# Performance work log

Hardware: AMD Instinct MI355X
Metric: run time of the kernel (lower is better)

The kernel has to match this reference:

```python
import jax, jax.numpy as jnp
import numpy as np

N = 50000        # nodes
E = 400000       # edges (avg degree 8)
F_IN = 128       # num_features
HID = 64         # hidden_channels
H = 4            # num_heads
D = HID // H     # headc = 16
C = 16           # num_classes
K_HOPS = 3
ALPHA = 0.1
CST = 1e-5


def setup_inputs() -> dict:
    key = jax.random.key(0)
    ks = jax.random.split(key, 16)
    s = 0.05
    x = jax.random.normal(ks[0], (N, F_IN), dtype=jnp.float32)
    edge_index = jax.random.randint(ks[1], (2, E), 0, N, dtype=jnp.int64)
    Wi = jax.random.normal(ks[2], (F_IN, HID), dtype=jnp.float32) * s
    bi = jnp.zeros((HID,), dtype=jnp.float32)
    Wq = jax.random.normal(ks[3], (HID, H * D), dtype=jnp.float32) * s
    bq = jnp.zeros((H * D,), dtype=jnp.float32)
    Wk = jax.random.normal(ks[4], (HID, H * D), dtype=jnp.float32) * s
    bk = jnp.zeros((H * D,), dtype=jnp.float32)
    Wv = jax.random.normal(ks[5], (HID, H * C), dtype=jnp.float32) * s
    bv = jnp.zeros((H * C,), dtype=jnp.float32)
    Wo = jax.random.normal(ks[6], (H * C, C), dtype=jnp.float32) * s
    bo = jnp.zeros((C,), dtype=jnp.float32)
    # hopwise/temp init as in the torch module (ind_gamma=True, gamma_softmax=True)
    hw = ALPHA * (1.0 - ALPHA) ** np.arange(K_HOPS + 1)
    hw[-1] = (1.0 - ALPHA) ** K_HOPS
    hopwise = jnp.asarray(hw, dtype=jnp.float32)
    temp = jax.random.uniform(ks[7], (H, K_HOPS + 1), dtype=jnp.float32)
    return {"x": x, "edge_index": edge_index, "Wi": Wi, "bi": bi, "Wq": Wq,
            "bq": bq, "Wk": Wk, "bk": bk, "Wv": Wv, "bv": bv, "Wo": Wo,
            "bo": bo, "hopwise": hopwise, "temp": temp}


def reference(x, edge_index, Wi, bi, Wq, bq, Wk, bk, Wv, bv, Wo, bo, hopwise, temp):
    # dropout p=0 (inference); input transform + relu
    h = jax.nn.relu(x @ Wi + bi)                       # (N, HID)
    Q = (1.0 + jax.nn.elu(h @ Wq + bq)).reshape(N, H, D)
    Kt = (1.0 + jax.nn.elu(h @ Wk + bk)).reshape(N, H, D)
    V = (h @ Wv + bv).reshape(N, H, C)
    M = jnp.einsum('nhi,nhj->nhij', Kt, V)             # (N, H, D, C)
    hidden = V * temp[:, 0][None, :, None]             # hop-0 term
    # NB: torch F.softmax(temp, dim=-2) normalizes over the HEAD axis
    layerwise = jax.nn.softmax(temp, axis=0)           # (H, K+1)
    src, dst = edge_index[0], edge_index[1]
    for hop in range(K_HOPS):
        M = jax.ops.segment_sum(M[src], dst, num_segments=N)
        Kt = jax.ops.segment_sum(Kt[src], dst, num_segments=N)
        Hm = jnp.einsum('nhi,nhij->nhj', Q, M)         # (N, H, C)
        den = jnp.einsum('nhi,nhi->nh', Q, Kt)[..., None] + CST
        gamma = hopwise[hop + 1] * layerwise[:, hop + 1][:, None]  # (H, 1)
        hidden = hidden + gamma * (Hm / den)
    # multi_concat=True path
    out = hidden.reshape(N, H * C) @ Wo + bo           # (N, C)
    return out
```

## Files before the change

kernel.cpp:

```cpp
#include <hip/hip_runtime.h>
#include <math.h>

#define F_IN 128
#define HID  64
#define NH   4
#define DD   16
#define CC   16
#define CSTE 1e-5f

typedef _Float16 h2     __attribute__((ext_vector_type(2)));
typedef float    f2     __attribute__((ext_vector_type(2)));
typedef short    short8 __attribute__((ext_vector_type(8)));
typedef float    f4v    __attribute__((ext_vector_type(4)));

#define WIT_LD 136
#define W2T_LD 72
#define H_LD   72

__device__ __forceinline__ unsigned short bf16r(float f) {
    unsigned int u = __builtin_bit_cast(unsigned int, f);
    unsigned int r = (u + 0x7FFFu + ((u >> 16) & 1u)) >> 16;
    return (unsigned short)r;
}

__device__ __forceinline__ int uni(int v) {
    return __builtin_amdgcn_readfirstlane(v);
}

__device__ __forceinline__ float fp8_to_f32(unsigned int b) {
    f2 v = __builtin_amdgcn_cvt_pk_f32_fp8((int)b, false);
    return v.x;
}
__device__ __forceinline__ f2 fp8x2_to_f32(unsigned int w) {
    return __builtin_amdgcn_cvt_pk_f32_fp8((int)w, false);
}
__device__ __forceinline__ f2 fp8x2_to_f32_hi(unsigned int w) {
    return __builtin_amdgcn_cvt_pk_f32_fp8((int)w, true);
}
__device__ __forceinline__ unsigned char f32_to_fp8(float f) {
    int w = __builtin_amdgcn_cvt_pk_fp8_f32(f, f, 0, false);
    return (unsigned char)(w & 0xff);
}

__device__ __forceinline__ float fp4_dec1(unsigned int n) {
    unsigned int e = (n >> 1) & 3u, m = n & 1u;
    float mag = (e == 0) ? 0.5f * (float)m
                         : (float)(1u << (e - 1)) * (1.0f + 0.5f * (float)m);
    return (n & 8u) ? -mag : mag;
}
__device__ __forceinline__ unsigned int fp4_enc1(float f) {
    unsigned int s = (f < 0.f) ? 8u : 0u;
    float a = fabsf(f);
    unsigned int m;
    if      (a < 0.25f) m = 0u;
    else if (a < 0.75f) m = 1u;
    else if (a < 1.25f) m = 2u;
    else if (a < 1.75f) m = 3u;
    else if (a < 2.5f)  m = 4u;
    else if (a < 3.5f)  m = 5u;
    else if (a < 5.0f)  m = 6u;
    else                m = 7u;
    return s | m;
}

#if __has_builtin(__builtin_amdgcn_cvt_scalef32_pk_f32_fp4) && __has_builtin(__builtin_amdgcn_cvt_scalef32_pk_fp4_f32)
#define HAS_FP4 1
#endif

__device__ __forceinline__ void fp4x16_dec2(uint2 w, f2* v) {
#ifdef HAS_FP4
    v[0] = __builtin_amdgcn_cvt_scalef32_pk_f32_fp4(w.x, 1.0f, 0);
    v[1] = __builtin_amdgcn_cvt_scalef32_pk_f32_fp4(w.x, 1.0f, 1);
    v[2] = __builtin_amdgcn_cvt_scalef32_pk_f32_fp4(w.x, 1.0f, 2);
    v[3] = __builtin_amdgcn_cvt_scalef32_pk_f32_fp4(w.x, 1.0f, 3);
    v[4] = __builtin_amdgcn_cvt_scalef32_pk_f32_fp4(w.y, 1.0f, 0);
    v[5] = __builtin_amdgcn_cvt_scalef32_pk_f32_fp4(w.y, 1.0f, 1);
    v[6] = __builtin_amdgcn_cvt_scalef32_pk_f32_fp4(w.y, 1.0f, 2);
    v[7] = __builtin_amdgcn_cvt_scalef32_pk_f32_fp4(w.y, 1.0f, 3);
#else
    #pragma unroll
    for (int j = 0; j < 4; ++j) {
        v[j].x     = fp4_dec1((w.x >> (8 * j)) & 0xFu);
        v[j].y     = fp4_dec1((w.x >> (8 * j + 4)) & 0xFu);
        v[4 + j].x = fp4_dec1((w.y >> (8 * j)) & 0xFu);
        v[4 + j].y = fp4_dec1((w.y >> (8 * j + 4)) & 0xFu);
    }
#endif
}

__device__ __forceinline__ uint2 fp4x16_enc(const float* v) {
#ifdef HAS_FP4
    unsigned int a = 0u, b = 0u;
    a = __builtin_amdgcn_cvt_scalef32_pk_fp4_f32(a, v[0],  v[1],  1.0f, 0);
    a = __builtin_amdgcn_cvt_scalef32_pk_fp4_f32(a, v[2],  v[3],  1.0f, 1);
    a = __builtin_amdgcn_cvt_scalef32_pk_fp4_f32(a, v[4],  v[5],  1.0f, 2);
    a = __builtin_amdgcn_cvt_scalef32_pk_fp4_f32(a, v[6],  v[7],  1.0f, 3);
    b = __builtin_amdgcn_cvt_scalef32_pk_fp4_f32(b, v[8],  v[9],  1.0f, 0);
    b = __builtin_amdgcn_cvt_scalef32_pk_fp4_f32(b, v[10], v[11], 1.0f, 1);
    b = __builtin_amdgcn_cvt_scalef32_pk_fp4_f32(b, v[12], v[13], 1.0f, 2);
    b = __builtin_amdgcn_cvt_scalef32_pk_fp4_f32(b, v[14], v[15], 1.0f, 3);
    return {a, b};
#else
    unsigned int a = 0u, b = 0u;
    #pragma unroll
    for (int j = 0; j < 8; ++j) {
        a |= fp4_enc1(v[j])     << (4 * j);
        b |= fp4_enc1(v[8 + j]) << (4 * j);
    }
    return {a, b};
#endif
}

__device__ __forceinline__ void store_m_row(
    uint2* __restrict__ Mout, unsigned short* __restrict__ SKout,
    int node, int lane, const float* u, float kacc)
{
    float rm = 0.f;
    #pragma unroll
    for (int j = 0; j < 16; ++j) rm = fmaxf(rm, fabsf(u[j]));
    unsigned char s8 = f32_to_fp8(rm * (1.0f / 6.0f));
    float se = fp8_to_f32((unsigned int)s8);
    float invs = (se > 0.f) ? (1.0f / se) : 0.f;
    float tq[16];
    #pragma unroll
    for (int j = 0; j < 16; ++j) tq[j] = u[j] * invs;
    Mout[(size_t)node * 64 + lane] = fp4x16_enc(tq);
    SKout[(size_t)node * 64 + lane] =
        (unsigned short)((unsigned short)s8 | ((unsigned short)f32_to_fp8(kacc) << 8));
}

__device__ __forceinline__ float gamma_for(const float* __restrict__ temp,
                                           const float* __restrict__ hopwise,
                                           int h, int hop) {
    float t0 = temp[0 * 4 + hop], t1 = temp[1 * 4 + hop];
    float t2 = temp[2 * 4 + hop], t3 = temp[3 * 4 + hop];
    float mx = fmaxf(fmaxf(t0, t1), fmaxf(t2, t3));
    float e0 = __expf(t0 - mx), e1 = __expf(t1 - mx);
    float e2 = __expf(t2 - mx), e3 = __expf(t3 - mx);
    float ssum = e0 + e1 + e2 + e3;
    float eh = (h == 0) ? e0 : (h == 1) ? e1 : (h == 2) ? e2 : e3;
    return hopwise[hop] * eh / ssum;
}

__device__ __forceinline__ void reduce_scatter16(float* u, int p) {
    #pragma unroll
    for (int k = 0; k < 4; ++k) {
        const int m = 1 << k;
        bool bit = (p >> k) & 1;
        const int n = 8 >> k;
        #pragma unroll
        for (int j = 0; j < n; ++j) {
            float give = bit ? u[2 * j]     : u[2 * j + 1];
            float keep = bit ? u[2 * j + 1] : u[2 * j];
            float got  = __shfl_xor(give, m, 64);
            u[j] = keep + got;
        }
    }
}

__device__ __forceinline__ float den16(float qd, float kacc) {
    float kq = qd * kacc;
    kq += __shfl_xor(kq, 1, 64);
    kq += __shfl_xor(kq, 2, 64);
    kq += __shfl_xor(kq, 4, 64);
    kq += __shfl_xor(kq, 8, 64);
    return kq + CSTE;
}

__device__ __forceinline__ void acc_edge23(f2* u2, float& kacc,
                                           uint2 w, unsigned int skraw) {
    f2 sk = fp8x2_to_f32(skraw);
    kacc += sk.y;
    f2 v[8];
    fp4x16_dec2(w, v);
    f2 s = {sk.x, sk.x};
    #pragma unroll
    for (int j = 0; j < 8; ++j) u2[j] = s * v[j] + u2[j];
}

__device__ __forceinline__ void acc_edge1(f2* u2, float& kacc,
                                          uint4 vw, unsigned int kraw) {
    float kk = fp8_to_f32(kraw);
    kacc += kk;
    f2 v[8];
    v[0] = fp8x2_to_f32(vw.x);  v[1] = fp8x2_to_f32_hi(vw.x);
    v[2] = fp8x2_to_f32(vw.y);  v[3] = fp8x2_to_f32_hi(vw.y);
    v[4] = fp8x2_to_f32(vw.z);  v[5] = fp8x2_to_f32_hi(vw.z);
    v[6] = fp8x2_to_f32(vw.w);  v[7] = fp8x2_to_f32_hi(vw.w);
    f2 s = {kk, kk};
    #pragma unroll
    for (int j = 0; j < 8; ++j) u2[j] = s * v[j] + u2[j];
}

__global__ __launch_bounds__(1024) void scan_a(const int* __restrict__ deg,
                                               int* __restrict__ offsets,
                                               int* __restrict__ bsum, int N) {
    __shared__ int wsum[16], woff[16];
    int lane = threadIdx.x & 63, w = threadIdx.x >> 6;
    int i0 = blockIdx.x * 4096 + (int)threadIdx.x * 4;
    int d0 = (i0 + 0 < N) ? deg[i0 + 0] : 0;
    int d1 = (i0 + 1 < N) ? deg[i0 + 1] : 0;
    int d2 = (i0 + 2 < N) ? deg[i0 + 2] : 0;
    int d3 = (i0 + 3 < N) ? deg[i0 + 3] : 0;
    int tsum = d0 + d1 + d2 + d3;
    int incl = tsum;
    #pragma unroll
    for (int m = 1; m < 64; m <<= 1) {
        int t = __shfl_up(incl, m, 64);
        if (lane >= m) incl += t;
    }
    if (lane == 63) wsum[w] = incl;
    __syncthreads();
    if (threadIdx.x == 0) {
        int r = 0;
        for (int k = 0; k < 16; ++k) { int t = wsum[k]; woff[k] = r; r += t; }
        bsum[blockIdx.x] = r;
    }
    __syncthreads();
    int excl = woff[w] + incl - tsum;
    if (i0 + 0 < N) offsets[i0 + 0] = excl;
    if (i0 + 1 < N) offsets[i0 + 1] = excl + d0;
    if (i0 + 2 < N) offsets[i0 + 2] = excl + d0 + d1;
    if (i0 + 3 < N) offsets[i0 + 3] = excl + d0 + d1 + d2;
}

__global__ void scan_c(int* __restrict__ offsets, const int* __restrict__ bsum,
                       int nb, int N) {
    int i = blockIdx.x * blockDim.x + threadIdx.x;
    if (i < N) {
        int bkt = i >> 12;
        int base = 0;
        for (int b = 0; b < bkt; ++b) base += bsum[b];
        offsets[i] += base;
    }
    if (i == 0) {
        int tot = 0;
        for (int b = 0; b < nb; ++b) tot += bsum[b];
        offsets[N] = tot;
    }
}

__global__ void scatter_kernel(const int* __restrict__ ei, const int* __restrict__ offsets,
                               int* __restrict__ cursor, int* __restrict__ csr, int E) {
    int e = blockIdx.x * blockDim.x + threadIdx.x;
    if (e < E) {
        int src = ei[e];
        int dst = ei[E + e];
        int pos = atomicAdd(&cursor[dst], 1);
        csr[offsets[dst] + pos] = src;
    }
}

__global__ __launch_bounds__(256) void qkv_count(
    const float* __restrict__ x,
    const float* __restrict__ Wi, const float* __restrict__ bi,
    const float* __restrict__ Wq, const float* __restrict__ bq,
    const float* __restrict__ Wk, const float* __restrict__ bk,
    const float* __restrict__ Wv, const float* __restrict__ bv,
    float* __restrict__ Q, unsigned char* __restrict__ VKq,
    _Float16* __restrict__ Vh,
    const int* __restrict__ ei, int* __restrict__ deg,
    int E, int qb, int N)
{
    __shared__ unsigned short wit[64 * WIT_LD];
    __shared__ unsigned short w2t[192 * W2T_LD];
    __shared__ unsigned short hlds[64 * H_LD];
    if ((int)blockIdx.x >= qb) {
        int e = ((int)blockIdx.x - qb) * 256 + (int)threadIdx.x;
        if (e < E) atomicAdd(&deg[ei[E + e]], 1);
        return;
    }
    int t = threadIdx.x;
    #pragma unroll
    for (int i = 0; i < 32; ++i) {
        int g = t + i * 256;
        wit[(g & 63) * WIT_LD + (g >> 6)] = bf16r(Wi[g]);
    }
    #pragma unroll
    for (int i = 0; i < 16; ++i) {
        int g = t + i * 256;
        int k = g >> 6, n = g & 63;
        w2t[(n      ) * W2T_LD + k] = bf16r(Wq[g]);
        w2t[(n +  64) * W2T_LD + k] = bf16r(Wk[g]);
        w2t[(n + 128) * W2T_LD + k] = bf16r(Wv[g]);
    }
    __syncthreads();

    int lane = t & 63, w = t >> 6;
    int p = lane & 15, quad = lane >> 4;
    int mbase = blockIdx.x * 64 + w * 16;

    short8 afrag[4];
    {
        int node = mbase + p;
        if (node >= N) node = N - 1;
        const float* xr = x + (size_t)node * F_IN + quad * 8;
        #pragma unroll
        for (int ks = 0; ks < 4; ++ks) {
            float4 a0 = *(const float4*)(xr + ks * 32);
            float4 a1 = *(const float4*)(xr + ks * 32 + 4);
            short8 f;
            f[0] = bf16r(a0.x); f[1] = bf16r(a0.y); f[2] = bf16r(a0.z); f[3] = bf16r(a0.w);
            f[4] = bf16r(a1.x); f[5] = bf16r(a1.y); f[6] = bf16r(a1.z); f[7] = bf16r(a1.w);
            afrag[ks] = f;
        }
    }
    #pragma unroll
    for (int nt = 0; nt < 4; ++nt) {
        f4v acc = {0.f, 0.f, 0.f, 0.f};
        #pragma unroll
        for (int ks = 0; ks < 4; ++ks) {
            short8 b = *(const short8*)&wit[(nt * 16 + p) * WIT_LD + ks * 32 + quad * 8];
            acc = __builtin_amdgcn_mfma_f32_16x16x32_bf16(afrag[ks], b, acc, 0, 0, 0);
        }
        float bb = bi[nt * 16 + p];
        #pragma unroll
        for (int r = 0; r < 4; ++r) {
            float hv = fmaxf(acc[r] + bb, 0.f);
            hlds[(w * 16 + quad * 4 + r) * H_LD + nt * 16 + p] = bf16r(hv);
        }
    }
    __syncthreads();

    short8 ha0 = *(const short8*)&hlds[(w * 16 + p) * H_LD + quad * 8];
    short8 ha1 = *(const short8*)&hlds[(w * 16 + p) * H_LD + 32 + quad * 8];
    int node_r = mbase + quad * 4;
    #pragma unroll
    for (int nt = 0; nt < 12; ++nt) {
        f4v acc = {0.f, 0.f, 0.f, 0.f};
        short8 b0 = *(const short8*)&w2t[(nt * 16 + p) * W2T_LD + quad * 8];
        short8 b1 = *(const short8*)&w2t[(nt * 16 + p) * W2T_LD + 32 + quad * 8];
        acc = __builtin_amdgcn_mfma_f32_16x16x32_bf16(ha0, b0, acc, 0, 0, 0);
        acc = __builtin_amdgcn_mfma_f32_16x16x32_bf16(ha1, b1, acc, 0, 0, 0);
        int col = nt * 16 + p;
        #pragma unroll
        for (int r = 0; r < 4; ++r) {
            int node = node_r + r;
            if (node >= N) continue;
            float v = acc[r];
            if (col < 64) {
                v += bq[col];
                Q[(size_t)node * 64 + col] = (v > 0.f) ? (1.f + v) : __expf(v);
            } else if (col < 128) {
                int c = col - 64;
                v += bk[c];
                float kv = (v > 0.f) ? (1.f + v) : __expf(v);
                VKq[(size_t)node * 128 + 64 + c] = f32_to_fp8(kv);
            } else {
                int c = col - 128;
                v += bv[c];
                Vh[(size_t)node * 64 + c] = (_Float16)v;
                VKq[(size_t)node * 128 + c] = f32_to_fp8(v);
            }
        }
    }
}


__global__ __launch_bounds__(256) void hop1_all(
    const float* __restrict__ Q, const unsigned char* __restrict__ VKq,
    const _Float16* __restrict__ Vh,
    const int* __restrict__ offsets, const int* __restrict__ csr,
    const float* __restrict__ temp, const float* __restrict__ hopwise,
    uint2* __restrict__ M1, unsigned short* __restrict__ SK1,
    float* __restrict__ hidden, int N)
{
    int lane = threadIdx.x & 63;
    int node = blockIdx.x * 4 + (threadIdx.x >> 6);
    if (node >= N) return;
    int h = lane >> 4;
    float gh = gamma_for(temp, hopwise, h, 1);
    float h0 = (float)Vh[(size_t)node * 64 + lane] * temp[h * 4];
    float qd = Q[(size_t)node * 64 + lane];
    f2 u2[8];
    #pragma unroll
    for (int j = 0; j < 8; ++j) u2[j] = f2{0.f, 0.f};
    float kacc = 0.f;
    int beg = uni(offsets[node]), end = uni(offsets[node + 1]);
    int t = beg;
    for (; t + 3 < end; t += 4) {
        int s0 = uni(csr[t]),     s1 = uni(csr[t + 1]);
        int s2 = uni(csr[t + 2]), s3 = uni(csr[t + 3]);
        const unsigned char* b0 = VKq + (size_t)s0 * 128;
        const unsigned char* b1 = VKq + (size_t)s1 * 128;
        const unsigned char* b2 = VKq + (size_t)s2 * 128;
        const unsigned char* b3 = VKq + (size_t)s3 * 128;
        uint4 v0 = *(const uint4*)(b0 + h * 16);
        uint4 v1 = *(const uint4*)(b1 + h * 16);
        uint4 v2 = *(const uint4*)(b2 + h * 16);
        uint4 v3 = *(const uint4*)(b3 + h * 16);
        unsigned char k0 = b0[64 + lane];
        unsigned char k1 = b1[64 + lane];
        unsigned char k2 = b2[64 + lane];
        unsigned char k3 = b3[64 + lane];
        acc_edge1(u2, kacc, v0, k0);
        acc_edge1(u2, kacc, v1, k1);
        acc_edge1(u2, kacc, v2, k2);
        acc_edge1(u2, kacc, v3, k3);
    }
    for (; t < end; ++t) {
        int s = uni(csr[t]);
        const unsigned char* b = VKq + (size_t)s * 128;
        uint4 vw = *(const uint4*)(b + h * 16);
        unsigned char kk = b[64 + lane];
        acc_edge1(u2, kacc, vw, kk);
    }
    float u[16];
    #pragma unroll
    for (int j = 0; j < 8; ++j) { u[2 * j] = u2[j].x; u[2 * j + 1] = u2[j].y; }
    store_m_row(M1, SK1, node, lane, u, kacc);
    #pragma unroll
    for (int j = 0; j < 16; ++j) u[j] *= qd;
    reduce_scatter16(u, lane & 15);
    float g = gh / den16(qd, kacc);
    hidden[(size_t)node * 64 + lane] = h0 + g * u[0];
}

template<bool STORE>
__global__ __launch_bounds__(256) void hop23_all(
    const float* __restrict__ Q, const uint2* __restrict__ Mprev,
    const unsigned short* __restrict__ SKprev,
    const int* __restrict__ offsets, const int* __restrict__ csr,
    const float* __restrict__ temp, const float* __restrict__ hopwise,
    uint2* __restrict__ Mnext, unsigned short* __restrict__ SKnext,
    float* __restrict__ hidden,
    const float* __restrict__ Wo, const float* __restrict__ bo,
    float* __restrict__ out, int N, int hop)
{
    int lane = threadIdx.x & 63;
    int node = blockIdx.x * 4 + (threadIdx.x >> 6);
    if (node >= N) return;
    float gh = gamma_for(temp, hopwise, lane >> 4, hop);
    float qd  = Q[(size_t)node * 64 + lane];
    float hv0 = STORE ? 0.f : hidden[(size_t)node * 64 + lane];
    f2 u2[8];
    #pragma unroll
    for (int j = 0; j < 8; ++j) u2[j] = f2{0.f, 0.f};
    float kacc = 0.f;
    int beg = uni(offsets[node]), end = uni(offsets[node + 1]);
    int t = beg;
    for (; t + 3 < end; t += 4) {
        int s0 = uni(csr[t]),     s1 = uni(csr[t + 1]);
        int s2 = uni(csr[t + 2]), s3 = uni(csr[t + 3]);
        uint2 w0 = Mprev[(size_t)s0 * 64 + lane];
        uint2 w1 = Mprev[(size_t)s1 * 64 + lane];
        uint2 w2 = Mprev[(size_t)s2 * 64 + lane];
        uint2 w3 = Mprev[(size_t)s3 * 64 + lane];
        unsigned short k0 = SKprev[(size_t)s0 * 64 + lane];
        unsigned short k1 = SKprev[(size_t)s1 * 64 + lane];
        unsigned short k2 = SKprev[(size_t)s2 * 64 + lane];
        unsigned short k3 = SKprev[(size_t)s3 * 64 + lane];
        acc_edge23(u2, kacc, w0, k0);
        acc_edge23(u2, kacc, w1, k1);
        acc_edge23(u2, kacc, w2, k2);
        acc_edge23(u2, kacc, w3, k3);
    }
    for (; t < end; ++t) {
        int sn = uni(csr[t]);
        uint2 w = Mprev[(size_t)sn * 64 + lane];
        unsigned short skr = SKprev[(size_t)sn * 64 + lane];
        acc_edge23(u2, kacc, w, skr);
    }
    float u[16];
    #pragma unroll
    for (int j = 0; j < 8; ++j) { u[2 * j] = u2[j].x; u[2 * j + 1] = u2[j].y; }
    if constexpr (STORE) store_m_row(Mnext, SKnext, node, lane, u, kacc);
    #pragma unroll
    for (int j = 0; j < 16; ++j) u[j] *= qd;
    reduce_scatter16(u, lane & 15);
    float g = gh / den16(qd, kacc);
    if constexpr (STORE) {
        hidden[(size_t)node * 64 + lane] += g * u[0];
    } else {
        float wrow[16];
        {
            const f4v* wp = (const f4v*)(Wo + (size_t)lane * 16);
            f4v a = wp[0], b = wp[1], c = wp[2], d = wp[3];
            wrow[0]=a[0]; wrow[1]=a[1]; wrow[2]=a[2]; wrow[3]=a[3];
            wrow[4]=b[0]; wrow[5]=b[1]; wrow[6]=b[2]; wrow[7]=b[3];
            wrow[8]=c[0]; wrow[9]=c[1]; wrow[10]=c[2]; wrow[11]=c[3];
            wrow[12]=d[0]; wrow[13]=d[1]; wrow[14]=d[2]; wrow[15]=d[3];
        }
        float hv = hv0 + g * u[0];
        float o[16];
        #pragma unroll
        for (int j = 0; j < 16; ++j) o[j] = hv * wrow[j];
        reduce_scatter16(o, lane & 15);
        float r = o[0];
        r += __shfl_xor(r, 16, 64);
        r += __shfl_xor(r, 32, 64);
        if (lane < 16) out[(size_t)node * 16 + lane] = r + bo[lane];
    }
}

extern "C" void kernel_launch(void* const* d_in, const int* in_sizes, int n_in,
                              void* d_out, int out_size, void* d_ws, size_t ws_size,
                              hipStream_t stream) {
    const float* x       = (const float*)d_in[0];
    const int*   ei      = (const int*)  d_in[1];
    const float* Wi      = (const float*)d_in[2];
    const float* bi      = (const float*)d_in[3];
    const float* Wq      = (const float*)d_in[4];
    const float* bq      = (const float*)d_in[5];
    const float* Wk      = (const float*)d_in[6];
    const float* bk      = (const float*)d_in[7];
    const float* Wv      = (const float*)d_in[8];
    const float* bv      = (const float*)d_in[9];
    const float* Wo      = (const float*)d_in[10];
    const float* bo      = (const float*)d_in[11];
    const float* hopwise = (const float*)d_in[12];
    const float* temp    = (const float*)d_in[13];

    const int N = in_sizes[0] / F_IN;
    const int E = in_sizes[1] / 2;

    char* ws = (char*)d_ws;
    size_t off = 0;
    auto take = [&](size_t bytes) -> char* {
        char* p = ws + off;
        off += (bytes + 255) & ~(size_t)255;
        return p;
    };
    float*          Q      = (float*)take((size_t)N * 64 * 4);
    _Float16*       Vh     = (_Float16*)take((size_t)N * 64 * 2);
    float*          hidden = (float*)take((size_t)N * 64 * 4);
    unsigned char*  VKq    = (unsigned char*)take((size_t)N * 128);
    unsigned short* SK1    = (unsigned short*)take((size_t)N * 64 * 2);
    unsigned short* SK2    = (unsigned short*)take((size_t)N * 64 * 2);
    int*            degcur = (int*)take((size_t)2 * N * 4);
    int*            offs   = (int*)take((size_t)(N + 1) * 4);
    int*            csr    = (int*)take((size_t)E * 4);
    int             nb     = (N + 4095) / 4096;
    int*            bsum   = (int*)take((size_t)nb * 4);
    uint2*          M1     = (uint2*)take((size_t)N * 512);
    uint2*          M2     = (uint2*)take((size_t)N * 512);

    int* deg    = degcur;
    int* cursor = degcur + N;

    hipMemsetAsync(degcur, 0, (size_t)2 * N * 4, stream);

    int eb = (E + 255) / 256;
    int qb = (N + 63) / 64;
    qkv_count<<<qb + eb, 256, 0, stream>>>(x, Wi, bi, Wq, bq, Wk, bk, Wv, bv,
                                           Q, VKq, Vh,
                                           ei, deg, E, qb, N);
    scan_a<<<nb, 1024, 0, stream>>>(deg, offs, bsum, N);
    scan_c<<<(N + 255) / 256, 256, 0, stream>>>(offs, bsum, nb, N);
    scatter_kernel<<<eb, 256, 0, stream>>>(ei, offs, cursor, csr, E);

    int nb4 = (N + 3) / 4;
    hop1_all<<<nb4, 256, 0, stream>>>(Q, VKq, Vh, offs, csr, temp, hopwise,
                                      M1, SK1, hidden, N);
    hop23_all<true ><<<nb4, 256, 0, stream>>>(Q, M1, SK1, offs, csr, temp, hopwise,
                                              M2, SK2, hidden,
                                              (const float*)nullptr, (const float*)nullptr,
                                              (float*)nullptr, N, 2);
    hop23_all<false><<<nb4, 256, 0, stream>>>(Q, M2, SK2, offs, csr, temp, hopwise,
                                              (uint2*)nullptr, (unsigned short*)nullptr,
                                              hidden, Wo, bo, (float*)d_out, N, 3);
}
```

Baseline: 288.7 us.

## Interleave packed M and scale/K arrays into single per-node rows, shrink blocks

```diff
diff --git a/kernel.cpp b/kernel.cpp
--- a/kernel.cpp
+++ b/kernel.cpp
@@ -7,6 +7,9 @@
 #define DD   16
 #define CC   16
 #define CSTE 1e-5f
+
+#define MROW 640
+#define SKOFF 512
 
 typedef _Float16 h2     __attribute__((ext_vector_type(2)));
 typedef float    f2     __attribute__((ext_vector_type(2)));
@@ -112,8 +115,7 @@
 }
 
 __device__ __forceinline__ void store_m_row(
-    uint2* __restrict__ Mout, unsigned short* __restrict__ SKout,
-    int node, int lane, const float* u, float kacc)
+    unsigned char* __restrict__ rowbase, int lane, const float* u, float kacc)
 {
     float rm = 0.f;
     #pragma unroll
@@ -124,8 +126,8 @@
     float tq[16];
     #pragma unroll
     for (int j = 0; j < 16; ++j) tq[j] = u[j] * invs;
-    Mout[(size_t)node * 64 + lane] = fp4x16_enc(tq);
-    SKout[(size_t)node * 64 + lane] =
+    *(uint2*)(rowbase + lane * 8) = fp4x16_enc(tq);
+    *(unsigned short*)(rowbase + SKOFF + lane * 2) =
         (unsigned short)((unsigned short)s8 | ((unsigned short)f32_to_fp8(kacc) << 8));
 }
 
@@ -357,16 +359,15 @@
 }
 
 
-__global__ __launch_bounds__(256) void hop1_all(
+__global__ __launch_bounds__(128) void hop1_all(
     const float* __restrict__ Q, const unsigned char* __restrict__ VKq,
     const _Float16* __restrict__ Vh,
     const int* __restrict__ offsets, const int* __restrict__ csr,
     const float* __restrict__ temp, const float* __restrict__ hopwise,
-    uint2* __restrict__ M1, unsigned short* __restrict__ SK1,
-    float* __restrict__ hidden, int N)
+    unsigned char* __restrict__ rows1, float* __restrict__ hidden, int N)
 {
     int lane = threadIdx.x & 63;
-    int node = blockIdx.x * 4 + (threadIdx.x >> 6);
+    int node = blockIdx.x * 2 + (threadIdx.x >> 6);
     if (node >= N) return;
     int h = lane >> 4;
     float gh = gamma_for(temp, hopwise, h, 1);
@@ -408,7 +409,7 @@
     float u[16];
     #pragma unroll
     for (int j = 0; j < 8; ++j) { u[2 * j] = u2[j].x; u[2 * j + 1] = u2[j].y; }
-    store_m_row(M1, SK1, node, lane, u, kacc);
+    store_m_row(rows1 + (size_t)node * MROW, lane, u, kacc);
     #pragma unroll
     for (int j = 0; j < 16; ++j) u[j] *= qd;
     reduce_scatter16(u, lane & 15);
@@ -417,18 +418,16 @@
 }
 
 template<bool STORE>
-__global__ __launch_bounds__(256) void hop23_all(
-    const float* __restrict__ Q, const uint2* __restrict__ Mprev,
-    const unsigned short* __restrict__ SKprev,
+__global__ __launch_bounds__(128) void hop23_all(
+    const float* __restrict__ Q, const unsigned char* __restrict__ rowsp,
     const int* __restrict__ offsets, const int* __restrict__ csr,
     const float* __restrict__ temp, const float* __restrict__ hopwise,
-    uint2* __restrict__ Mnext, unsigned short* __restrict__ SKnext,
-    float* __restrict__ hidden,
+    unsigned char* __restrict__ rowsn, float* __restrict__ hidden,
     const float* __restrict__ Wo, const float* __restrict__ bo,
     float* __restrict__ out, int N, int hop)
 {
     int lane = threadIdx.x & 63;
-    int node = blockIdx.x * 4 + (threadIdx.x >> 6);
+    int node = blockIdx.x * 2 + (threadIdx.x >> 6);
     if (node >= N) return;
     float gh = gamma_for(temp, hopwise, lane >> 4, hop);
     float qd  = Q[(size_t)node * 64 + lane];
@@ -437,19 +436,24 @@
     #pragma unroll
     for (int j = 0; j < 8; ++j) u2[j] = f2{0.f, 0.f};
     float kacc = 0.f;
+    int mo = lane * 8, so = SKOFF + lane * 2;
     int beg = uni(offsets[node]), end = uni(offsets[node + 1]);
     int t = beg;
     for (; t + 3 < end; t += 4) {
         int s0 = uni(csr[t]),     s1 = uni(csr[t + 1]);
         int s2 = uni(csr[t + 2]), s3 = uni(csr[t + 3]);
-        uint2 w0 = Mprev[(size_t)s0 * 64 + lane];
-        uint2 w1 = Mprev[(size_t)s1 * 64 + lane];
-        uint2 w2 = Mprev[(size_t)s2 * 64 + lane];
-        uint2 w3 = Mprev[(size_t)s3 * 64 + lane];
-        unsigned short k0 = SKprev[(size_t)s0 * 64 + lane];
-        unsigned short k1 = SKprev[(size_t)s1 * 64 + lane];
-        unsigned short k2 = SKprev[(size_t)s2 * 64 + lane];
-        unsigned short k3 = SKprev[(size_t)s3 * 64 + lane];
+        const unsigned char* r0 = rowsp + (size_t)s0 * MROW;
+        const unsigned char* r1 = rowsp + (size_t)s1 * MROW;
+        const unsigned char* r2 = rowsp + (size_t)s2 * MROW;
+        const unsigned char* r3 = rowsp + (size_t)s3 * MROW;
+        uint2 w0 = *(const uint2*)(r0 + mo);
+        uint2 w1 = *(const uint2*)(r1 + mo);
+        uint2 w2 = *(const uint2*)(r2 + mo);
+        uint2 w3 = *(const uint2*)(r3 + mo);
+        unsigned short k0 = *(const unsigned short*)(r0 + so);
+        unsigned short k1 = *(const unsigned short*)(r1 + so);
+        unsigned short k2 = *(const unsigned short*)(r2 + so);
+        unsigned short k3 = *(const unsigned short*)(r3 + so);
         acc_edge23(u2, kacc, w0, k0);
         acc_edge23(u2, kacc, w1, k1);
         acc_edge23(u2, kacc, w2, k2);
@@ -457,14 +461,15 @@
     }
     for (; t < end; ++t) {
         int sn = uni(csr[t]);
-        uint2 w = Mprev[(size_t)sn * 64 + lane];
-        unsigned short skr = SKprev[(size_t)sn * 64 + lane];
+        const unsigned char* r = rowsp + (size_t)sn * MROW;
+        uint2 w = *(const uint2*)(r + mo);
+        unsigned short skr = *(const unsigned short*)(r + so);
         acc_edge23(u2, kacc, w, skr);
     }
     float u[16];
     #pragma unroll
     for (int j = 0; j < 8; ++j) { u[2 * j] = u2[j].x; u[2 * j + 1] = u2[j].y; }
-    if constexpr (STORE) store_m_row(Mnext, SKnext, node, lane, u, kacc);
+    if constexpr (STORE) store_m_row(rowsn + (size_t)node * MROW, lane, u, kacc);
     #pragma unroll
     for (int j = 0; j < 16; ++j) u[j] *= qd;
     reduce_scatter16(u, lane & 15);
@@ -525,15 +530,13 @@
     _Float16*       Vh     = (_Float16*)take((size_t)N * 64 * 2);
     float*          hidden = (float*)take((size_t)N * 64 * 4);
     unsigned char*  VKq    = (unsigned char*)take((size_t)N * 128);
-    unsigned short* SK1    = (unsigned short*)take((size_t)N * 64 * 2);
-    unsigned short* SK2    = (unsigned short*)take((size_t)N * 64 * 2);
     int*            degcur = (int*)take((size_t)2 * N * 4);
     int*            offs   = (int*)take((size_t)(N + 1) * 4);
     int*            csr    = (int*)take((size_t)E * 4);
     int             nb     = (N + 4095) / 4096;
     int*            bsum   = (int*)take((size_t)nb * 4);
-    uint2*          M1     = (uint2*)take((size_t)N * 512);
-    uint2*          M2     = (uint2*)take((size_t)N * 512);
+    unsigned char*  rows1  = (unsigned char*)take((size_t)N * MROW);
+    unsigned char*  rows2  = (unsigned char*)take((size_t)N * MROW);
 
     int* deg    = degcur;
     int* cursor = degcur + N;
@@ -549,14 +552,14 @@
     scan_c<<<(N + 255) / 256, 256, 0, stream>>>(offs, bsum, nb, N);
     scatter_kernel<<<eb, 256, 0, stream>>>(ei, offs, cursor, csr, E);
 
-    int nb4 = (N + 3) / 4;
-    hop1_all<<<nb4, 256, 0, stream>>>(Q, VKq, Vh, offs, csr, temp, hopwise,
-                                      M1, SK1, hidden, N);
-    hop23_all<true ><<<nb4, 256, 0, stream>>>(Q, M1, SK1, offs, csr, temp, hopwise,
-                                              M2, SK2, hidden,
+    int nb2 = (N + 1) / 2;
+    hop1_all<<<nb2, 128, 0, stream>>>(Q, VKq, Vh, offs, csr, temp, hopwise,
+                                      rows1, hidden, N);
+    hop23_all<true ><<<nb2, 128, 0, stream>>>(Q, rows1, offs, csr, temp, hopwise,
+                                              rows2, hidden,
                                               (const float*)nullptr, (const float*)nullptr,
                                               (float*)nullptr, N, 2);
-    hop23_all<false><<<nb4, 256, 0, stream>>>(Q, M2, SK2, offs, csr, temp, hopwise,
-                                              (uint2*)nullptr, (unsigned short*)nullptr,
-                                              hidden, Wo, bo, (float*)d_out, N, 3);
-}
+    hop23_all<false><<<nb2, 128, 0, stream>>>(Q, rows2, offs, csr, temp, hopwise,
+                                              (unsigned char*)nullptr, hidden,
+                                              Wo, bo, (float*)d_out, N, 3);
+}
```

Measured after the change: 285.0 us. No clear change (-1.3%).
